# Performance work log

Hardware: AMD Instinct MI355X
Metric: run time of the kernel (lower is better)

The kernel has to match this reference:

```python
import jax, jax.numpy as jnp
import numpy as np

N = 50000
NEG_SLOPE = 0.2


def _glorot(key, shape):
    fan_in = shape[0]
    return jax.random.normal(key, shape, dtype=jnp.float32) / np.sqrt(fan_in)


def setup_inputs() -> dict:
    key = jax.random.key(0)
    ks = jax.random.split(key, 12)
    F_IN, H, C = 128, 128, 2
    E = 800000
    x = jax.random.normal(ks[0], (N, F_IN), dtype=jnp.float32)
    edge_index = jax.random.randint(ks[1], (2, E), 0, N, dtype=jnp.int64)
    return {
        "x": x,
        "edge_index": edge_index,
        # GATv2Conv 1: num_features -> hidden_units
        "Wl1": _glorot(ks[2], (F_IN, H)),
        "Wr1": _glorot(ks[3], (F_IN, H)),
        "att1": _glorot(ks[4], (H,)),
        "b1": jnp.zeros((H,), dtype=jnp.float32),
        # Linear skip 1
        "Wlin1": _glorot(ks[5], (F_IN, H)),
        "blin1": jnp.zeros((H,), dtype=jnp.float32),
        # GATv2Conv 2: hidden_units -> num_classes
        "Wl2": _glorot(ks[6], (H, C)),
        "Wr2": _glorot(ks[7], (H, C)),
        "att2": _glorot(ks[8], (C,)),
        "b2": jnp.zeros((C,), dtype=jnp.float32),
        # Linear skip 2
        "Wlin2": _glorot(ks[9], (H, C)),
        "blin2": jnp.zeros((C,), dtype=jnp.float32),
    }


def _gatv2_conv(x, src, dst, Wl, Wr, att, bias):
    # PyG GATv2Conv, heads=1: score = att . leaky_relu(Wl x_j + Wr x_i)
    xl = x @ Wl  # source-side transform [N, H]
    xr = x @ Wr  # target-side transform [N, H]
    m = xl[src] + xr[dst]  # [E, H]
    m = jnp.where(m > 0, m, NEG_SLOPE * m)
    e = m @ att  # [E]
    # segment softmax over incoming edges of each target node
    emax = jax.ops.segment_max(e, dst, num_segments=N)
    a = jnp.exp(e - emax[dst])
    denom = jax.ops.segment_sum(a, dst, num_segments=N)
    alpha = a / denom[dst]  # [E]
    out = jax.ops.segment_sum(alpha[:, None] * xl[src], dst, num_segments=N)
    return out + bias


def reference(x, edge_index, Wl1, Wr1, att1, b1, Wlin1, blin1,
              Wl2, Wr2, att2, b2, Wlin2, blin2):
    # add self loops (PyG default add_self_loops=True)
    loops = jnp.arange(N, dtype=edge_index.dtype)
    src = jnp.concatenate([edge_index[0], loops])
    dst = jnp.concatenate([edge_index[1], loops])

    h = _gatv2_conv(x, src, dst, Wl1, Wr1, att1, b1) + (x @ Wlin1 + blin1)
    h = jax.nn.relu(h)
    out = _gatv2_conv(h, src, dst, Wl2, Wr2, att2, b2) + (h @ Wlin2 + blin2)
    return (jax.nn.log_softmax(out, axis=1), edge_index)
```

## Files before the change

kernel.cpp:

```cpp
#include <hip/hip_runtime.h>
#include <math.h>

#define N_NODES 50000
#define F_IN 128
#define E_RAW 800000
#define E_TOT (E_RAW + N_NODES)
#define NEG_SLOPE 0.2f

#define TRR 128
#define TCC 64
#define KBB 32
#define XP33 33

__global__ __launch_bounds__(256, 4) void gemm1_kernel(
    const float* __restrict__ x,
    const float* __restrict__ Wl, const float* __restrict__ Wr,
    const float* __restrict__ Wlin,
    float* __restrict__ XL, float* __restrict__ XR, float* __restrict__ LIN)
{
    __shared__ float XS[TRR][XP33];
    __shared__ float WS[KBB][TCC];

    const int t  = threadIdx.x;
    const int tx = t & 15;
    const int ty = t >> 4;

    const int r0   = blockIdx.x * TRR;
    const int half = blockIdx.y & 1;
    const int mat  = blockIdx.y >> 1;
    const int cs0  = half * 64;

    const float* Wsel = (mat == 0) ? Wl : (mat == 1) ? Wr : Wlin;
    float*       Osel = (mat == 0) ? XL : (mat == 1) ? XR : LIN;

    const int sx_k4  = t & 7;
    const int sx_row = t >> 3;

    float acc[8][4];
    #pragma unroll
    for (int r = 0; r < 8; ++r)
        #pragma unroll
        for (int c = 0; c < 4; ++c) acc[r][c] = 0.f;

    for (int kc = 0; kc < 128; kc += KBB) {
        #pragma unroll
        for (int i = 0; i < 4; ++i) {
            const int row = sx_row + i * 32;
            const int gr  = r0 + row;
            float4 v = (gr < N_NODES)
                ? *(const float4*)(x + (size_t)gr * 128 + kc + sx_k4 * 4)
                : make_float4(0.f, 0.f, 0.f, 0.f);
            XS[row][sx_k4 * 4 + 0] = v.x;
            XS[row][sx_k4 * 4 + 1] = v.y;
            XS[row][sx_k4 * 4 + 2] = v.z;
            XS[row][sx_k4 * 4 + 3] = v.w;
        }
        #pragma unroll
        for (int i = 0; i < 2; ++i) {
            const int wk = (t >> 4) + i * 16;
            float4 wv = *(const float4*)(Wsel + (size_t)(kc + wk) * 128 + cs0 + tx * 4);
            *(float4*)&WS[wk][tx * 4] = wv;
        }
        __syncthreads();

        #pragma unroll 8
        for (int k = 0; k < KBB; ++k) {
            const float4 wv = *(const float4*)&WS[k][tx * 4];
            float xv[8];
            #pragma unroll
            for (int r = 0; r < 8; ++r) xv[r] = XS[ty * 8 + r][k];
            #pragma unroll
            for (int r = 0; r < 8; ++r) {
                acc[r][0] = fmaf(xv[r], wv.x, acc[r][0]);
                acc[r][1] = fmaf(xv[r], wv.y, acc[r][1]);
                acc[r][2] = fmaf(xv[r], wv.z, acc[r][2]);
                acc[r][3] = fmaf(xv[r], wv.w, acc[r][3]);
            }
        }
        __syncthreads();
    }

    #pragma unroll
    for (int r = 0; r < 8; ++r) {
        const int grow = r0 + ty * 8 + r;
        if (grow < N_NODES) {
            float4 o = make_float4(acc[r][0], acc[r][1], acc[r][2], acc[r][3]);
            *(float4*)(Osel + (size_t)grow * 128 + cs0 + tx * 4) = o;
        }
    }
}

__global__ __launch_bounds__(256) void hist_kernel(
    const int* __restrict__ eidx, int* __restrict__ counts)
{
    const int e = blockIdx.x * blockDim.x + threadIdx.x;
    if (e >= E_TOT) return;
    const int d = (e < E_RAW) ? eidx[E_RAW + e] : e - E_RAW;
    atomicAdd(&counts[d], 1);
}

__global__ __launch_bounds__(1024) void scan_kernel(
    const int* __restrict__ counts, int* __restrict__ rowptr, int* __restrict__ cursor)
{
    __shared__ int wsum[16];
    __shared__ int carry_s;
    const int tid = threadIdx.x, lane = tid & 63, wv = tid >> 6;
    if (tid == 0) carry_s = 0;
    __syncthreads();

    for (int base = 0; base < N_NODES; base += 1024) {
        const int i = base + tid;
        const int orig = (i < N_NODES) ? counts[i] : 0;
        int v = orig;
        #pragma unroll
        for (int off = 1; off < 64; off <<= 1) {
            int t = __shfl_up(v, off);
            if (lane >= off) v += t;
        }
        if (lane == 63) wsum[wv] = v;
        __syncthreads();
        if (wv == 0) {
            int s = (lane < 16) ? wsum[lane] : 0;
            #pragma unroll
            for (int off = 1; off < 16; off <<= 1) {
                int t = __shfl_up(s, off);
                if (lane >= off) s += t;
            }
            if (lane < 16) wsum[lane] = s;
        }
        __syncthreads();
        const int carry = carry_s;
        const int woff  = (wv == 0) ? 0 : wsum[wv - 1];
        const int excl  = carry + woff + v - orig;
        if (i < N_NODES) { rowptr[i] = excl; cursor[i] = excl; }
        __syncthreads();
        if (tid == 0) carry_s += wsum[15];
        __syncthreads();
    }
    if (threadIdx.x == 0) rowptr[N_NODES] = carry_s;
}

__global__ __launch_bounds__(256) void scatter_kernel(
    const int* __restrict__ eidx, int* __restrict__ cursor, int* __restrict__ csr_src)
{
    const int e = blockIdx.x * blockDim.x + threadIdx.x;
    if (e >= E_TOT) return;
    int s, d;
    if (e < E_RAW) { s = eidx[e]; d = eidx[E_RAW + e]; }
    else           { s = d = e - E_RAW; }
    const int pos = atomicAdd(&cursor[d], 1);
    csr_src[pos] = s;
}

__global__ __launch_bounds__(256) void fused1_kernel(
    const float* __restrict__ xl, const float* __restrict__ xr,
    const float* __restrict__ lin,
    const int* __restrict__ rowptr, const int* __restrict__ csr_src,
    const float* __restrict__ att, const float* __restrict__ b1,
    const float* __restrict__ blin1,
    const float* __restrict__ Wl2, const float* __restrict__ Wr2,
    const float* __restrict__ Wlin2,
    float* __restrict__ XL2, float* __restrict__ XR2, float* __restrict__ LIN2)
{
    const int gid  = blockIdx.x * blockDim.x + threadIdx.x;
    const int d    = gid >> 6;
    const int lane = gid & 63;
    if (d >= N_NODES) return;
    const int grp = lane >> 4;
    const int sub = lane & 15;

    const int r0 = rowptr[d], r1 = rowptr[d + 1];

    const float4 xr0 = *(const float4*)(xr + (size_t)d * 128 + sub * 8);
    const float4 xr1 = *(const float4*)(xr + (size_t)d * 128 + sub * 8 + 4);
    const float4 at0 = *(const float4*)(att + sub * 8);
    const float4 at1 = *(const float4*)(att + sub * 8 + 4);

    float num[8] = {0.f,0.f,0.f,0.f,0.f,0.f,0.f,0.f};
    float den = 0.f;

    for (int j = r0; j < r1; j += 4) {
        const int e  = j + grp;
        const int ee = (e < E_TOT) ? e : (E_TOT - 1);
        const int s  = csr_src[ee];
        const float4 a0 = *(const float4*)(xl + (size_t)s * 128 + sub * 8);
        const float4 a1 = *(const float4*)(xl + (size_t)s * 128 + sub * 8 + 4);

        float m, v = 0.f;
        m = a0.x + xr0.x; m = m > 0.f ? m : NEG_SLOPE * m; v = fmaf(m, at0.x, v);
        m = a0.y + xr0.y; m = m > 0.f ? m : NEG_SLOPE * m; v = fmaf(m, at0.y, v);
        m = a0.z + xr0.z; m = m > 0.f ? m : NEG_SLOPE * m; v = fmaf(m, at0.z, v);
        m = a0.w + xr0.w; m = m > 0.f ? m : NEG_SLOPE * m; v = fmaf(m, at0.w, v);
        m = a1.x + xr1.x; m = m > 0.f ? m : NEG_SLOPE * m; v = fmaf(m, at1.x, v);
        m = a1.y + xr1.y; m = m > 0.f ? m : NEG_SLOPE * m; v = fmaf(m, at1.y, v);
        m = a1.z + xr1.z; m = m > 0.f ? m : NEG_SLOPE * m; v = fmaf(m, at1.z, v);
        m = a1.w + xr1.w; m = m > 0.f ? m : NEG_SLOPE * m; v = fmaf(m, at1.w, v);

        v += __shfl_xor(v, 1);
        v += __shfl_xor(v, 2);
        v += __shfl_xor(v, 4);
        v += __shfl_xor(v, 8);

        const float ex = (e < r1) ? __expf(v) : 0.f;
        den += ex;
        num[0] = fmaf(ex, a0.x, num[0]);
        num[1] = fmaf(ex, a0.y, num[1]);
        num[2] = fmaf(ex, a0.z, num[2]);
        num[3] = fmaf(ex, a0.w, num[3]);
        num[4] = fmaf(ex, a1.x, num[4]);
        num[5] = fmaf(ex, a1.y, num[5]);
        num[6] = fmaf(ex, a1.z, num[6]);
        num[7] = fmaf(ex, a1.w, num[7]);
    }

    den += __shfl_xor(den, 16);
    den += __shfl_xor(den, 32);
    #pragma unroll
    for (int i = 0; i < 8; ++i) {
        num[i] += __shfl_xor(num[i], 16);
        num[i] += __shfl_xor(num[i], 32);
    }

    const float inv = 1.f / den;
    const float4 l0  = *(const float4*)(lin   + (size_t)d * 128 + sub * 8);
    const float4 l1  = *(const float4*)(lin   + (size_t)d * 128 + sub * 8 + 4);
    const float4 bb0 = *(const float4*)(b1    + sub * 8);
    const float4 bb1 = *(const float4*)(b1    + sub * 8 + 4);
    const float4 bl0 = *(const float4*)(blin1 + sub * 8);
    const float4 bl1 = *(const float4*)(blin1 + sub * 8 + 4);
    float h0 = fmaf(num[0], inv, bb0.x) + l0.x + bl0.x;
    float h1 = fmaf(num[1], inv, bb0.y) + l0.y + bl0.y;
    float h2 = fmaf(num[2], inv, bb0.z) + l0.z + bl0.z;
    float h3 = fmaf(num[3], inv, bb0.w) + l0.w + bl0.w;
    float h4 = fmaf(num[4], inv, bb1.x) + l1.x + bl1.x;
    float h5 = fmaf(num[5], inv, bb1.y) + l1.y + bl1.y;
    float h6 = fmaf(num[6], inv, bb1.z) + l1.z + bl1.z;
    float h7 = fmaf(num[7], inv, bb1.w) + l1.w + bl1.w;
    h0 = h0 > 0.f ? h0 : 0.f;  h1 = h1 > 0.f ? h1 : 0.f;
    h2 = h2 > 0.f ? h2 : 0.f;  h3 = h3 > 0.f ? h3 : 0.f;
    h4 = h4 > 0.f ? h4 : 0.f;  h5 = h5 > 0.f ? h5 : 0.f;
    h6 = h6 > 0.f ? h6 : 0.f;  h7 = h7 > 0.f ? h7 : 0.f;

    float pl0, pl1, pr0, pr1, pn0, pn1;
    {
        const float4 a = ((const float4*)Wl2)[sub*4+0];
        const float4 b = ((const float4*)Wl2)[sub*4+1];
        const float4 c = ((const float4*)Wl2)[sub*4+2];
        const float4 e4= ((const float4*)Wl2)[sub*4+3];
        pl0 = h0*a.x + h1*a.z + h2*b.x + h3*b.z + h4*c.x + h5*c.z + h6*e4.x + h7*e4.z;
        pl1 = h0*a.y + h1*a.w + h2*b.y + h3*b.w + h4*c.y + h5*c.w + h6*e4.y + h7*e4.w;
    }
    {
        const float4 a = ((const float4*)Wr2)[sub*4+0];
        const float4 b = ((const float4*)Wr2)[sub*4+1];
        const float4 c = ((const float4*)Wr2)[sub*4+2];
        const float4 e4= ((const float4*)Wr2)[sub*4+3];
        pr0 = h0*a.x + h1*a.z + h2*b.x + h3*b.z + h4*c.x + h5*c.z + h6*e4.x + h7*e4.z;
        pr1 = h0*a.y + h1*a.w + h2*b.y + h3*b.w + h4*c.y + h5*c.w + h6*e4.y + h7*e4.w;
    }
    {
        const float4 a = ((const float4*)Wlin2)[sub*4+0];
        const float4 b = ((const float4*)Wlin2)[sub*4+1];
        const float4 c = ((const float4*)Wlin2)[sub*4+2];
        const float4 e4= ((const float4*)Wlin2)[sub*4+3];
        pn0 = h0*a.x + h1*a.z + h2*b.x + h3*b.z + h4*c.x + h5*c.z + h6*e4.x + h7*e4.z;
        pn1 = h0*a.y + h1*a.w + h2*b.y + h3*b.w + h4*c.y + h5*c.w + h6*e4.y + h7*e4.w;
    }
    #pragma unroll
    for (int off = 1; off < 16; off <<= 1) {
        pl0 += __shfl_xor(pl0, off); pl1 += __shfl_xor(pl1, off);
        pr0 += __shfl_xor(pr0, off); pr1 += __shfl_xor(pr1, off);
        pn0 += __shfl_xor(pn0, off); pn1 += __shfl_xor(pn1, off);
    }
    if (lane == 0) {
        XL2[d*2+0]  = pl0; XL2[d*2+1]  = pl1;
        XR2[d*2+0]  = pr0; XR2[d*2+1]  = pr1;
        LIN2[d*2+0] = pn0; LIN2[d*2+1] = pn1;
    }
}

__global__ __launch_bounds__(256) void fused2_kernel(
    const float* __restrict__ XL2, const float* __restrict__ XR2,
    const float* __restrict__ LIN2,
    const int* __restrict__ rowptr, const int* __restrict__ csr_src,
    const float* __restrict__ att2, const float* __restrict__ b2,
    const float* __restrict__ blin2,
    float* __restrict__ out)
{
    const int gid = blockIdx.x * blockDim.x + threadIdx.x;
    const int d   = gid >> 4;
    const int l16 = gid & 15;
    if (d >= N_NODES) return;

    const int r0 = rowptr[d], r1 = rowptr[d + 1];
    const float2 xrv = *(const float2*)(XR2 + (size_t)d * 2);
    const float a0 = att2[0], a1 = att2[1];

    float num0 = 0.f, num1 = 0.f, den = 0.f;
    for (int j = r0 + l16; j < r1; j += 16) {
        const int s = csr_src[j];
        const float2 l = *(const float2*)(XL2 + (size_t)s * 2);
        float m0 = l.x + xrv.x, m1 = l.y + xrv.y;
        m0 = m0 > 0.f ? m0 : NEG_SLOPE * m0;
        m1 = m1 > 0.f ? m1 : NEG_SLOPE * m1;
        const float ex = __expf(fmaf(m0, a0, m1 * a1));
        den += ex;
        num0 = fmaf(ex, l.x, num0);
        num1 = fmaf(ex, l.y, num1);
    }
    #pragma unroll
    for (int off = 1; off < 16; off <<= 1) {
        den  += __shfl_xor(den,  off);
        num0 += __shfl_xor(num0, off);
        num1 += __shfl_xor(num1, off);
    }
    if (l16 == 0) {
        const float inv = 1.f / den;
        const float o0 = num0 * inv + b2[0] + LIN2[d*2+0] + blin2[0];
        const float o1 = num1 * inv + b2[1] + LIN2[d*2+1] + blin2[1];
        const float mx  = fmaxf(o0, o1);
        const float lse = mx + logf(__expf(o0 - mx) + __expf(o1 - mx));
        out[d*2+0] = o0 - lse;
        out[d*2+1] = o1 - lse;
    }
}

__global__ __launch_bounds__(256) void copy_eidx_kernel(
    const int* __restrict__ eidx, float* __restrict__ out)
{
    const int i = blockIdx.x * blockDim.x + threadIdx.x;
    if (i >= 2 * E_RAW) return;
    out[i] = (float)eidx[i];
}

extern "C" void kernel_launch(void* const* d_in, const int* in_sizes, int n_in,
                              void* d_out, int out_size, void* d_ws, size_t ws_size,
                              hipStream_t stream)
{
    const float* x      = (const float*)d_in[0];
    const int*   eidx   = (const int*)  d_in[1];
    const float* Wl1    = (const float*)d_in[2];
    const float* Wr1    = (const float*)d_in[3];
    const float* att1   = (const float*)d_in[4];
    const float* b1     = (const float*)d_in[5];
    const float* Wlin1  = (const float*)d_in[6];
    const float* blin1  = (const float*)d_in[7];
    const float* Wl2    = (const float*)d_in[8];
    const float* Wr2    = (const float*)d_in[9];
    const float* att2   = (const float*)d_in[10];
    const float* b2     = (const float*)d_in[11];
    const float* Wlin2  = (const float*)d_in[12];
    const float* blin2  = (const float*)d_in[13];

    float* out = (float*)d_out;

    float* ws     = (float*)d_ws;
    float* XL     = ws;
    float* XR     = ws + 6400000;
    float* LIN    = ws + 12800000;
    int*   counts = (int*)(ws + 19200000);
    int*   rowptr = counts + 50000;
    int*   csr    = rowptr + 50001;
    float* XL2    = out + 100000;
    float* XR2    = out + 200000;
    float* LIN2   = out + 300000;

    {
        dim3 grid((N_NODES + TRR - 1) / TRR, 6);
        gemm1_kernel<<<grid, 256, 0, stream>>>(x, Wl1, Wr1, Wlin1, XL, XR, LIN);
    }

    hipMemsetAsync(counts, 0, N_NODES * sizeof(int), stream);
    hist_kernel<<<(E_TOT + 255) / 256, 256, 0, stream>>>(eidx, counts);
    scan_kernel<<<1, 1024, 0, stream>>>(counts, rowptr, counts);
    scatter_kernel<<<(E_TOT + 255) / 256, 256, 0, stream>>>(eidx, counts, csr);

    {
        const int blocks = (N_NODES * 64 + 255) / 256;
        fused1_kernel<<<blocks, 256, 0, stream>>>(XL, XR, LIN, rowptr, csr,
                                                  att1, b1, blin1,
                                                  Wl2, Wr2, Wlin2,
                                                  XL2, XR2, LIN2);
    }

    {
        const int blocks = (N_NODES * 16 + 255) / 256;
        fused2_kernel<<<blocks, 256, 0, stream>>>(XL2, XR2, LIN2, rowptr, csr,
                                                  att2, b2, blin2, out);
    }

    {
        const int blocks = (2 * E_RAW + 255) / 256;
        copy_eidx_kernel<<<blocks, 256, 0, stream>>>(eidx, out + (size_t)N_NODES * 2);
    }
}
```

Measured before the change: 392.5 us.

## Parallelize CSR prefix scan across blocks and vectorize GEMM shared-memory reads

Replaces the single-block serial-loop exclusive scan over node degrees with a three-kernel reduce-then-scan-then-apply scheme spread over 196 blocks, with a separate cursor buffer. The point is to remove a long single-workgroup latency stage from the CSR build. The first GEMM's shared tile is re-padded to a stride of 36 so it can take float4 stores and loads, and the k loop is unrolled in groups of four to cut LDS instruction count. The cost is two extra kernel launches and a different LDS bank-conflict pattern.

Result: faster. 352.6 us (-10.2%).

```diff
diff --git a/kernel.cpp b/kernel.cpp
--- a/kernel.cpp
+++ b/kernel.cpp
@@ -6,11 +6,12 @@
 #define E_RAW 800000
 #define E_TOT (E_RAW + N_NODES)
 #define NEG_SLOPE 0.2f
+#define NPART 196
 
 #define TRR 128
 #define TCC 64
 #define KBB 32
-#define XP33 33
+#define XST 36
 
 __global__ __launch_bounds__(256, 4) void gemm1_kernel(
     const float* __restrict__ x,
@@ -18,7 +19,7 @@
     const float* __restrict__ Wlin,
     float* __restrict__ XL, float* __restrict__ XR, float* __restrict__ LIN)
 {
-    __shared__ float XS[TRR][XP33];
+    __shared__ float XS[TRR][XST];
     __shared__ float WS[KBB][TCC];
 
     const int t  = threadIdx.x;
@@ -50,10 +51,7 @@
             float4 v = (gr < N_NODES)
                 ? *(const float4*)(x + (size_t)gr * 128 + kc + sx_k4 * 4)
                 : make_float4(0.f, 0.f, 0.f, 0.f);
-            XS[row][sx_k4 * 4 + 0] = v.x;
-            XS[row][sx_k4 * 4 + 1] = v.y;
-            XS[row][sx_k4 * 4 + 2] = v.z;
-            XS[row][sx_k4 * 4 + 3] = v.w;
+            *(float4*)&XS[row][sx_k4 * 4] = v;
         }
         #pragma unroll
         for (int i = 0; i < 2; ++i) {
@@ -63,18 +61,31 @@
         }
         __syncthreads();
 
-        #pragma unroll 8
-        for (int k = 0; k < KBB; ++k) {
-            const float4 wv = *(const float4*)&WS[k][tx * 4];
-            float xv[8];
-            #pragma unroll
-            for (int r = 0; r < 8; ++r) xv[r] = XS[ty * 8 + r][k];
+        #pragma unroll 1
+        for (int kb = 0; kb < 8; ++kb) {
+            const float4 wv0 = *(const float4*)&WS[kb * 4 + 0][tx * 4];
+            const float4 wv1 = *(const float4*)&WS[kb * 4 + 1][tx * 4];
+            const float4 wv2 = *(const float4*)&WS[kb * 4 + 2][tx * 4];
+            const float4 wv3 = *(const float4*)&WS[kb * 4 + 3][tx * 4];
             #pragma unroll
             for (int r = 0; r < 8; ++r) {
-                acc[r][0] = fmaf(xv[r], wv.x, acc[r][0]);
-                acc[r][1] = fmaf(xv[r], wv.y, acc[r][1]);
-                acc[r][2] = fmaf(xv[r], wv.z, acc[r][2]);
-                acc[r][3] = fmaf(xv[r], wv.w, acc[r][3]);
+                const float4 xq = *(const float4*)&XS[ty * 8 + r][kb * 4];
+                acc[r][0] = fmaf(xq.x, wv0.x, acc[r][0]);
+                acc[r][1] = fmaf(xq.x, wv0.y, acc[r][1]);
+                acc[r][2] = fmaf(xq.x, wv0.z, acc[r][2]);
+                acc[r][3] = fmaf(xq.x, wv0.w, acc[r][3]);
+                acc[r][0] = fmaf(xq.y, wv1.x, acc[r][0]);
+                acc[r][1] = fmaf(xq.y, wv1.y, acc[r][1]);
+                acc[r][2] = fmaf(xq.y, wv1.z, acc[r][2]);
+                acc[r][3] = fmaf(xq.y, wv1.w, acc[r][3]);
+                acc[r][0] = fmaf(xq.z, wv2.x, acc[r][0]);
+                acc[r][1] = fmaf(xq.z, wv2.y, acc[r][1]);
+                acc[r][2] = fmaf(xq.z, wv2.z, acc[r][2]);
+                acc[r][3] = fmaf(xq.z, wv2.w, acc[r][3]);
+                acc[r][0] = fmaf(xq.w, wv3.x, acc[r][0]);
+                acc[r][1] = fmaf(xq.w, wv3.y, acc[r][1]);
+                acc[r][2] = fmaf(xq.w, wv3.z, acc[r][2]);
+                acc[r][3] = fmaf(xq.w, wv3.w, acc[r][3]);
             }
         }
         __syncthreads();
@@ -99,45 +110,61 @@
     atomicAdd(&counts[d], 1);
 }
 
-__global__ __launch_bounds__(1024) void scan_kernel(
-    const int* __restrict__ counts, int* __restrict__ rowptr, int* __restrict__ cursor)
-{
-    __shared__ int wsum[16];
-    __shared__ int carry_s;
-    const int tid = threadIdx.x, lane = tid & 63, wv = tid >> 6;
-    if (tid == 0) carry_s = 0;
+__global__ __launch_bounds__(256) void scan_partial_kernel(
+    const int* __restrict__ counts, int* __restrict__ part)
+{
+    const int i = blockIdx.x * 256 + threadIdx.x;
+    int v = (i < N_NODES) ? counts[i] : 0;
+    #pragma unroll
+    for (int off = 32; off > 0; off >>= 1) v += __shfl_xor(v, off);
+    __shared__ int ws[4];
+    if ((threadIdx.x & 63) == 0) ws[threadIdx.x >> 6] = v;
     __syncthreads();
-
-    for (int base = 0; base < N_NODES; base += 1024) {
-        const int i = base + tid;
-        const int orig = (i < N_NODES) ? counts[i] : 0;
-        int v = orig;
-        #pragma unroll
-        for (int off = 1; off < 64; off <<= 1) {
-            int t = __shfl_up(v, off);
-            if (lane >= off) v += t;
-        }
-        if (lane == 63) wsum[wv] = v;
-        __syncthreads();
-        if (wv == 0) {
-            int s = (lane < 16) ? wsum[lane] : 0;
-            #pragma unroll
-            for (int off = 1; off < 16; off <<= 1) {
-                int t = __shfl_up(s, off);
-                if (lane >= off) s += t;
-            }
-            if (lane < 16) wsum[lane] = s;
-        }
-        __syncthreads();
-        const int carry = carry_s;
-        const int woff  = (wv == 0) ? 0 : wsum[wv - 1];
-        const int excl  = carry + woff + v - orig;
-        if (i < N_NODES) { rowptr[i] = excl; cursor[i] = excl; }
-        __syncthreads();
-        if (tid == 0) carry_s += wsum[15];
-        __syncthreads();
-    }
-    if (threadIdx.x == 0) rowptr[N_NODES] = carry_s;
+    if (threadIdx.x == 0) part[blockIdx.x] = ws[0] + ws[1] + ws[2] + ws[3];
+}
+
+__global__ __launch_bounds__(256) void scan_part_kernel(int* __restrict__ part)
+{
+    const int t = threadIdx.x, lane = t & 63, w = t >> 6;
+    int v = (t < NPART) ? part[t] : 0;
+    const int orig = v;
+    #pragma unroll
+    for (int off = 1; off < 64; off <<= 1) {
+        int u = __shfl_up(v, off);
+        if (lane >= off) v += u;
+    }
+    __shared__ int ws[4];
+    if (lane == 63) ws[w] = v;
+    __syncthreads();
+    int add = 0;
+    for (int j = 0; j < w; ++j) add += ws[j];
+    if (t < NPART) part[t] = add + v - orig;
+}
+
+__global__ __launch_bounds__(256) void scan_apply_kernel(
+    const int* __restrict__ counts, const int* __restrict__ part,
+    int* __restrict__ rowptr, int* __restrict__ cursor)
+{
+    const int i = blockIdx.x * 256 + threadIdx.x;
+    const int t = threadIdx.x, lane = t & 63, w = t >> 6;
+    int v = (i < N_NODES) ? counts[i] : 0;
+    const int orig = v;
+    #pragma unroll
+    for (int off = 1; off < 64; off <<= 1) {
+        int u = __shfl_up(v, off);
+        if (lane >= off) v += u;
+    }
+    __shared__ int ws[4];
+    if (lane == 63) ws[w] = v;
+    __syncthreads();
+    int add = part[blockIdx.x];
+    for (int j = 0; j < w; ++j) add += ws[j];
+    if (i < N_NODES) {
+        const int e = add + v - orig;
+        rowptr[i] = e;
+        cursor[i] = e;
+    }
+    if (i == 0) rowptr[N_NODES] = E_TOT;
 }
 
 __global__ __launch_bounds__(256) void scatter_kernel(
@@ -361,6 +388,8 @@
     int*   counts = (int*)(ws + 19200000);
     int*   rowptr = counts + 50000;
     int*   csr    = rowptr + 50001;
+    int*   part   = csr + E_TOT;
+    int*   cursor = part + NPART;
     float* XL2    = out + 100000;
     float* XR2    = out + 200000;
     float* LIN2   = out + 300000;
@@ -372,8 +401,10 @@
 
     hipMemsetAsync(counts, 0, N_NODES * sizeof(int), stream);
     hist_kernel<<<(E_TOT + 255) / 256, 256, 0, stream>>>(eidx, counts);
-    scan_kernel<<<1, 1024, 0, stream>>>(counts, rowptr, counts);
-    scatter_kernel<<<(E_TOT + 255) / 256, 256, 0, stream>>>(eidx, counts, csr);
+    scan_partial_kernel<<<NPART, 256, 0, stream>>>(counts, part);
+    scan_part_kernel<<<1, 256, 0, stream>>>(part);
+    scan_apply_kernel<<<NPART, 256, 0, stream>>>(counts, part, rowptr, cursor);
+    scatter_kernel<<<(E_TOT + 255) / 256, 256, 0, stream>>>(eidx, cursor, csr);
 
     {
         const int blocks = (N_NODES * 64 + 255) / 256;
```
